# Performance work log

Measured on AMD Instinct MI355X. Metric: run time of the kernel, lower is better.

Reference implementation:

```python
import jax, jax.numpy as jnp
import numpy as np

H = 2048          # hidden size
N_HEADS = 16
HEAD_DIM = H // N_HEADS   # 128
ATTN_SCALE = 8.0          # attention_scale > 1.0 -> custom max-subtract path
B, S = 2, 2048


def setup_inputs() -> dict:
    key = jax.random.key(0)
    k1, k2, k3, k4, k5 = jax.random.split(key, 5)
    hidden_states = jax.random.normal(k1, (B, S, H), dtype=jnp.float32)
    # causal left-to-right multiplicative mask, broadcast over batch and heads
    ltor_mask = jnp.tril(jnp.ones((S, S), dtype=jnp.float32))[None, None]
    std = 0.02
    W_qkv = jax.random.normal(k2, (H, 3 * H), dtype=jnp.float32) * std
    b_qkv = jnp.zeros((3 * H,), dtype=jnp.float32)
    W_out = jax.random.normal(k3, (H, H), dtype=jnp.float32) * std
    b_out = jnp.zeros((H,), dtype=jnp.float32)
    return {"hidden_states": hidden_states, "ltor_mask": ltor_mask,
            "W_qkv": W_qkv, "b_qkv": b_qkv, "W_out": W_out, "b_out": b_out}


def reference(hidden_states, ltor_mask, W_qkv, b_qkv, W_out, b_out):
    b, s, h = hidden_states.shape
    # fused QKV projection: [b, s, 3h]
    qkv = jnp.einsum('bsh,hk->bsk', hidden_states, W_qkv) + b_qkv
    q, k, v = jnp.split(qkv, 3, axis=-1)
    # [b, s, h] -> [b, n, s, hn]
    def to_heads(t):
        return t.reshape(b, s, N_HEADS, HEAD_DIM).transpose(0, 2, 1, 3)
    q, k, v = to_heads(q), to_heads(k), to_heads(v)
    # custom scale: q / sqrt(scale), k / sqrt(hn * scale)
    inv = 1.0 / (ATTN_SCALE * np.sqrt(np.float32(HEAD_DIM)))
    scores = jnp.einsum('bnqd,bnkd->bnqk', q, k) * jnp.float32(inv)
    # multiplicative mask BEFORE max-subtract (zeroes masked positions)
    scores = scores * ltor_mask
    # attention_scale > 1.0 path: subtract row max, re-multiply by scale
    scores = (scores - jnp.max(scores, axis=-1, keepdims=True)) * jnp.float32(ATTN_SCALE)
    # additive large-negative fill on masked entries
    scores = scores + jnp.float32(-65504.0) * (1.0 - ltor_mask)
    probs = jax.nn.softmax(scores, axis=-1)
    ctx = jnp.einsum('bnqk,bnkd->bnqd', probs, v)
    ctx = ctx.transpose(0, 2, 1, 3).reshape(b, s, h)
    out = jnp.einsum('bsh,hk->bsk', ctx, W_out) + b_out
    return out
```

## Files before the change

### kernel.cpp

```cpp
#include <hip/hip_runtime.h>

#define S_LEN 2048
#define HDIM  2048
#define NHEADS 16
#define DHEAD 128
#define BATCH 2
#define MROWS (BATCH * S_LEN)
#define QKVN  (3 * HDIM)

typedef _Float16 f16;
typedef _Float16 f16x8 __attribute__((ext_vector_type(8)));
typedef _Float16 f16x4 __attribute__((ext_vector_type(4)));
typedef float    f32x4 __attribute__((ext_vector_type(4)));
typedef float    f32x16 __attribute__((ext_vector_type(16)));

typedef const __attribute__((address_space(1))) void* gas_ptr;
typedef __attribute__((address_space(3))) void*       las_ptr;

#define MFMA16(a, b, c)  __builtin_amdgcn_mfma_f32_16x16x32_f16(a, b, c, 0, 0, 0)
#define MFMA32(a, b, c)  __builtin_amdgcn_mfma_f32_32x32x16_f16(a, b, c, 0, 0, 0)

__device__ __forceinline__ void gl_lds16(const f16* g, f16* lds_wave_base) {
  __builtin_amdgcn_global_load_lds((gas_ptr)g, (las_ptr)lds_wave_base, 16, 0, 0);
}


__device__ __forceinline__ void transpose_tile(const float* __restrict__ W,
                                               f16* __restrict__ Wb,
                                               int K, int N, int k0, int n0,
                                               float* tile ) {
  int tr = threadIdx.x >> 4;
  int tc = (threadIdx.x & 15) * 4;
  int KT = K >> 5;
#pragma unroll
  for (int rr = 0; rr < 4; ++rr) {
    int r = rr * 16 + tr;
    float4 v = *(const float4*)(W + (size_t)(k0 + r) * N + n0 + tc);
    tile[r * 65 + tc + 0] = v.x; tile[r * 65 + tc + 1] = v.y;
    tile[r * 65 + tc + 2] = v.z; tile[r * 65 + tc + 3] = v.w;
  }
  __syncthreads();
#pragma unroll
  for (int rr = 0; rr < 4; ++rr) {
    int r = rr * 16 + tr;
    int n = n0 + r;
    int kBase = k0 + tc;
    f16x4 o;
#pragma unroll
    for (int c = 0; c < 4; ++c) o[c] = (f16)tile[(tc + c) * 65 + r];
    int nt = n >> 7, nn = n & 127;
    int kt = kBase >> 5, kc = (kBase >> 3) & 3, j = kBase & 7;
    *(f16x4*)(Wb + ((size_t)nt * KT + kt) * 4096 + (kc * 128 + nn) * 8 + j) = o;
  }
}

__global__ __launch_bounds__(256) void prep_kernel(const float* __restrict__ X,
                                                   f16* __restrict__ Xb,
                                                   const float* __restrict__ Wqkv,
                                                   f16* __restrict__ Wqkvb,
                                                   const float* __restrict__ Wout,
                                                   f16* __restrict__ Woutb) {
  __shared__ float tile[64 * 65];
  int bz = blockIdx.x;
  if (bz < 2048) {
    int kt = bz & 63, rt = bz >> 6;
    int t = threadIdx.x;
    int m = t >> 1, half = t & 1;
    const float* src = X + (size_t)(rt * 128 + m) * HDIM + kt * 32 + half * 16;
    float4 v0 = ((const float4*)src)[0];
    float4 v1 = ((const float4*)src)[1];
    float4 v2 = ((const float4*)src)[2];
    float4 v3 = ((const float4*)src)[3];
    f16x8 a = {(f16)v0.x, (f16)v0.y, (f16)v0.z, (f16)v0.w,
               (f16)v1.x, (f16)v1.y, (f16)v1.z, (f16)v1.w};
    f16x8 b = {(f16)v2.x, (f16)v2.y, (f16)v2.z, (f16)v2.w,
               (f16)v3.x, (f16)v3.y, (f16)v3.z, (f16)v3.w};
    f16* dst = Xb + ((size_t)rt * 64 + kt) * 4096 + ((half * 2) * 128 + m) * 8;
    *(f16x8*)dst = a;
    *(f16x8*)(dst + 1024) = b;
  } else if (bz < 5120) {
    int u = bz - 2048;
    int nx = u % 96, ky = u / 96;
    transpose_tile(Wqkv, Wqkvb, HDIM, QKVN, ky * 64, nx * 64, tile);
  } else {
    int u = bz - 5120;
    int nx = u & 31, ky = u >> 5;
    transpose_tile(Wout, Woutb, HDIM, HDIM, ky * 64, nx * 64, tile);
  }
}

__global__ __launch_bounds__(512, 2) void gemm_qkv_kernel(const f16* __restrict__ Ablk,
                                                          const f16* __restrict__ Bblk,
                                                          const float* __restrict__ bias,
                                                          f16* __restrict__ Qr,
                                                          f16* __restrict__ KB,
                                                          f16* __restrict__ VB) {
  __shared__ f16 As[3][2][4096];
  __shared__ f16 Bs[3][3][4096];
  const int tid = threadIdx.x;
  const int lane = tid & 63, wv = tid >> 6;
  const int lhi = lane >> 4, llo = lane & 15;
  const int wr = wv >> 2, wc = wv & 3;

  int lin = blockIdx.x + 16 * blockIdx.y;
  int xcd = lin & 7, slot = lin >> 3;
  int bx = (xcd & 3) * 4 + (slot & 3);
  int by = (xcd >> 2) * 8 + (slot >> 2);

  const int KT = HDIM >> 5;
  const f16* Ab0 = Ablk + (size_t)(2 * by)     * KT * 4096;
  const f16* Ab1 = Ablk + (size_t)(2 * by + 1) * KT * 4096;
  const f16* Bb0 = Bblk + (size_t)(3 * bx)     * KT * 4096;
  const f16* Bb1 = Bblk + (size_t)(3 * bx + 1) * KT * 4096;
  const f16* Bb2 = Bblk + (size_t)(3 * bx + 2) * KT * 4096;

  f32x4 acc[8][6];
#pragma unroll
  for (int i = 0; i < 8; ++i)
#pragma unroll
    for (int j = 0; j < 6; ++j) acc[i][j] = (f32x4){0.f, 0.f, 0.f, 0.f};

  auto stA = [&](int bufi, int kt) {
    gl_lds16(Ab0 + (size_t)kt * 4096 + tid * 8, &As[bufi][0][0] + wv * 512);
    gl_lds16(Ab1 + (size_t)kt * 4096 + tid * 8, &As[bufi][1][0] + wv * 512);
  };
  auto stB = [&](int bufi, int kt) {
    gl_lds16(Bb0 + (size_t)kt * 4096 + tid * 8, &Bs[bufi][0][0] + wv * 512);
    gl_lds16(Bb1 + (size_t)kt * 4096 + tid * 8, &Bs[bufi][1][0] + wv * 512);
    gl_lds16(Bb2 + (size_t)kt * 4096 + tid * 8, &Bs[bufi][2][0] + wv * 512);
  };
  auto rdB = [&](int bufi, int j) -> f16x8 {
    int cg = wc * 96 + j * 16;
    return *(const f16x8*)(&Bs[bufi][cg >> 7][0] + (lhi * 128 + (cg & 127) + llo) * 8);
  };

  stA(0, 0); stB(0, 0);
  stA(1, 1); stB(1, 1);

  for (int t = 0; t < KT; ++t) {
    const int buf = t % 3;
    const bool st = (t + 2 < KT);
    const int nb = (t + 2) % 3;

    if (t + 1 < KT) asm volatile("s_waitcnt vmcnt(5)" ::: "memory");
    else            asm volatile("s_waitcnt vmcnt(0)" ::: "memory");
    __builtin_amdgcn_s_barrier();

    const f16* Ah = &As[buf][wr][0];
    f16x8 afr[8], bA, bB;

#pragma unroll
    for (int i = 0; i < 8; ++i)
      afr[i] = *(const f16x8*)(Ah + (lhi * 128 + i * 16 + llo) * 8);
    bA = rdB(buf, 0); bB = rdB(buf, 1);
    if (st) stA(nb, t + 2);
    __builtin_amdgcn_s_barrier();
    asm volatile("s_waitcnt lgkmcnt(0)" ::: "memory");
    __builtin_amdgcn_s_setprio(1);
#pragma unroll
    for (int i = 0; i < 8; ++i) acc[i][0] = MFMA16(afr[i], bA, acc[i][0]);
#pragma unroll
    for (int i = 0; i < 8; ++i) acc[i][1] = MFMA16(afr[i], bB, acc[i][1]);
    __builtin_amdgcn_s_setprio(0);

    bA = rdB(buf, 2); bB = rdB(buf, 3);
    if (st) stB(nb, t + 2);
    __builtin_amdgcn_s_barrier();
    asm volatile("s_waitcnt lgkmcnt(0)" ::: "memory");
    __builtin_amdgcn_s_setprio(1);
#pragma unroll
    for (int i = 0; i < 8; ++i) acc[i][2] = MFMA16(afr[i], bA, acc[i][2]);
#pragma unroll
    for (int i = 0; i < 8; ++i) acc[i][3] = MFMA16(afr[i], bB, acc[i][3]);
    __builtin_amdgcn_s_setprio(0);

    bA = rdB(buf, 4); bB = rdB(buf, 5);
    __builtin_amdgcn_s_barrier();
    asm volatile("s_waitcnt lgkmcnt(0)" ::: "memory");
    __builtin_amdgcn_s_setprio(1);
#pragma unroll
    for (int i = 0; i < 8; ++i) acc[i][4] = MFMA16(afr[i], bA, acc[i][4]);
#pragma unroll
    for (int i = 0; i < 8; ++i) acc[i][5] = MFMA16(afr[i], bB, acc[i][5]);
    __builtin_amdgcn_s_setprio(0);
  }

#pragma unroll
  for (int j = 0; j < 6; ++j) {
    int col = bx * 384 + wc * 96 + j * 16 + llo;
    float bv = bias[col];
#pragma unroll
    for (int i = 0; i < 8; ++i) {
      int rowb = by * 256 + wr * 128 + i * 16 + lhi * 4;
      int region = col >> 11;
      if (region == 0) {
#pragma unroll
        for (int r = 0; r < 4; ++r)
          Qr[(size_t)(rowb + r) * HDIM + col] = (f16)(acc[i][j][r] + bv);
      } else if (region == 1) {
        int cK = col - HDIM;
        int hd = cK >> 7, d = cK & 127, g = d >> 3, dj = d & 7;
#pragma unroll
        for (int r = 0; r < 4; ++r) {
          int row = rowb + r;
          int b = row >> 11, s = row & 2047;
          int kt2 = s >> 6, key = s & 63;
          size_t addr = ((((size_t)(b * 16 + hd) * 32 + kt2) * 16 + g) * 64 + key) * 8 + dj;
          KB[addr] = (f16)(acc[i][j][r] + bv);
        }
      } else {
        int cV = col - 2 * HDIM;
        int hd = cV >> 7, d = cV & 127;
        int row = rowb;
        int b = row >> 11, s = row & 2047;
        int kt2 = s >> 6, key = s & 63;
        int kg = key >> 3, kj = key & 7;
        f16x4 pv = {(f16)(acc[i][j][0] + bv), (f16)(acc[i][j][1] + bv),
                    (f16)(acc[i][j][2] + bv), (f16)(acc[i][j][3] + bv)};
        size_t addr = ((((size_t)(b * 16 + hd) * 32 + kt2) * 8 + kg) * 128 + d) * 8 + kj;
        *(f16x4*)(VB + addr) = pv;
      }
    }
  }
}

__global__ __launch_bounds__(512, 2) void gemm_out_kernel(const f16* __restrict__ Ablk,
                                                          const f16* __restrict__ Bblk,
                                                          f16* __restrict__ Cpart) {
  __shared__ f16 As[4][2][4096];
  __shared__ f16 Bs[4][2][4096];
  const int tid = threadIdx.x;
  const int lane = tid & 63, wv = tid >> 6;
  const int lhi = lane >> 4, llo = lane & 15;
  const int wr = wv >> 2, wc = wv & 3;

  int lin = blockIdx.x + 8 * (blockIdx.y + 16 * blockIdx.z);
  int xcd = lin & 7, slot = lin >> 3;
  int bx = slot & 7;
  int by = (xcd >> 1) * 4 + (slot >> 3);
  int bz = xcd & 1;

  const int KT = HDIM >> 5;
  const int ntiles = KT >> 1;
  const int t0 = bz * ntiles;

  const f16* Ab0 = Ablk + ((size_t)(2 * by)     * KT + t0) * 4096;
  const f16* Ab1 = Ablk + ((size_t)(2 * by + 1) * KT + t0) * 4096;
  const f16* Bb0 = Bblk + ((size_t)(2 * bx)     * KT + t0) * 4096;
  const f16* Bb1 = Bblk + ((size_t)(2 * bx + 1) * KT + t0) * 4096;

  f32x4 acc[8][4];
#pragma unroll
  for (int i = 0; i < 8; ++i)
#pragma unroll
    for (int j = 0; j < 4; ++j) acc[i][j] = (f32x4){0.f, 0.f, 0.f, 0.f};

  auto stA = [&](int bufi, int kt) {
    gl_lds16(Ab0 + (size_t)kt * 4096 + tid * 8, &As[bufi][0][0] + wv * 512);
    gl_lds16(Ab1 + (size_t)kt * 4096 + tid * 8, &As[bufi][1][0] + wv * 512);
  };
  auto stB = [&](int bufi, int kt) {
    gl_lds16(Bb0 + (size_t)kt * 4096 + tid * 8, &Bs[bufi][0][0] + wv * 512);
    gl_lds16(Bb1 + (size_t)kt * 4096 + tid * 8, &Bs[bufi][1][0] + wv * 512);
  };

#pragma unroll
  for (int u = 0; u < 3; ++u) { stA(u, u); stB(u, u); }

  for (int t = 0; t < ntiles; ++t) {
    const int buf = t & 3;
    const bool st = (t + 3 < ntiles);
    const int nb = (t + 3) & 3, ntile = t + 3;

    if (t + 2 < ntiles)      asm volatile("s_waitcnt vmcnt(8)" ::: "memory");
    else if (t + 1 < ntiles) asm volatile("s_waitcnt vmcnt(4)" ::: "memory");
    else                     asm volatile("s_waitcnt vmcnt(0)" ::: "memory");
    __builtin_amdgcn_s_barrier();

    const f16* Ah = &As[buf][wr][0];
    const f16* Bh = &Bs[buf][wc >> 1][0];
    f16x8 bfr[4], afr[4];

#pragma unroll
    for (int j = 0; j < 4; ++j)
      bfr[j] = *(const f16x8*)(Bh + (lhi * 128 + (wc & 1) * 64 + j * 16 + llo) * 8);
#pragma unroll
    for (int i = 0; i < 4; ++i)
      afr[i] = *(const f16x8*)(Ah + (lhi * 128 + i * 16 + llo) * 8);
    if (st) stA(nb, ntile);
    __builtin_amdgcn_s_barrier();
    asm volatile("s_waitcnt lgkmcnt(0)" ::: "memory");
    __builtin_amdgcn_s_setprio(1);
#pragma unroll
    for (int i = 0; i < 4; ++i)
#pragma unroll
      for (int j = 0; j < 4; ++j) acc[i][j] = MFMA16(afr[i], bfr[j], acc[i][j]);
    __builtin_amdgcn_s_setprio(0);
    __builtin_amdgcn_s_barrier();

#pragma unroll
    for (int i = 0; i < 4; ++i)
      afr[i] = *(const f16x8*)(Ah + (lhi * 128 + (i + 4) * 16 + llo) * 8);
    if (st) stB(nb, ntile);
    __builtin_amdgcn_s_barrier();
    asm volatile("s_waitcnt lgkmcnt(0)" ::: "memory");
    __builtin_amdgcn_s_setprio(1);
#pragma unroll
    for (int i = 0; i < 4; ++i)
#pragma unroll
      for (int j = 0; j < 4; ++j) acc[i + 4][j] = MFMA16(afr[i], bfr[j], acc[i + 4][j]);
    __builtin_amdgcn_s_setprio(0);
  }

#pragma unroll
  for (int j = 0; j < 4; ++j) {
    int col = bx * 256 + wc * 64 + j * 16 + llo;
#pragma unroll
    for (int i = 0; i < 8; ++i) {
      int rowb = by * 256 + wr * 128 + i * 16 + lhi * 4;
      size_t zoff = (size_t)bz * MROWS * HDIM;
#pragma unroll
      for (int r = 0; r < 4; ++r)
        Cpart[zoff + (size_t)(rowb + r) * HDIM + col] = (f16)acc[i][j][r];
    }
  }
}

__global__ __launch_bounds__(256) void merge_out_kernel(const f16* __restrict__ Cpart,
                                                        const float* __restrict__ bias,
                                                        float* __restrict__ out) {
  int t = blockIdx.x * 256 + threadIdx.x;
  int col8 = (t & 255) * 8;
  int row = t >> 8;
  size_t base = (size_t)row * HDIM + col8;
  const size_t MN = (size_t)MROWS * HDIM;
  f16x8 a = *(const f16x8*)(Cpart + base);
  f16x8 b = *(const f16x8*)(Cpart + MN + base);
  float4 b0 = *(const float4*)(bias + col8);
  float4 b1 = *(const float4*)(bias + col8 + 4);
  float4 o0 = {(float)a[0] + (float)b[0] + b0.x, (float)a[1] + (float)b[1] + b0.y,
               (float)a[2] + (float)b[2] + b0.z, (float)a[3] + (float)b[3] + b0.w};
  float4 o1 = {(float)a[4] + (float)b[4] + b1.x, (float)a[5] + (float)b[5] + b1.y,
               (float)a[6] + (float)b[6] + b1.z, (float)a[7] + (float)b[7] + b1.w};
  *(float4*)(out + base) = o0;
  *(float4*)(out + base + 4) = o1;
}

__global__ __launch_bounds__(512, 1) void attn_kernel(const f16* __restrict__ Qr,
                                                      const f16* __restrict__ KB,
                                                      const f16* __restrict__ VB,
                                                      f16* __restrict__ CTXb) {
  __shared__ f16 Ks[2][1024 * 8];
  __shared__ f16 Vs[2][1024 * 8];
  __shared__ f16 Ps[8][32 * 72];

  int tid = threadIdx.x, lane = tid & 63, w = tid >> 6;
  int l5 = lane & 31, hl = lane >> 5;

  int lin = blockIdx.x + 8 * blockIdx.y;
  int xcd = lin & 7, slot = lin >> 3;
  int bh = xcd + 8 * (slot & 3);
  int pr = slot >> 2;
  int qt = (w < 4) ? pr : (15 - pr);
  int b = bh >> 4, hd = bh & 15;
  int ktmax = 32 - 2 * pr;

  int qbase = qt * 128 + (w & 3) * 32;
  int qrow = qbase + l5;

  const f16* qp = Qr + (size_t)(b * S_LEN + qrow) * HDIM + hd * DHEAD + hl * 8;
  f16x8 qf[8];
#pragma unroll
  for (int s8 = 0; s8 < 8; ++s8) qf[s8] = *(const f16x8*)(qp + s8 * 16);

  f32x16 oac[4];
#pragma unroll
  for (int mt = 0; mt < 4; ++mt)
#pragma unroll
    for (int r = 0; r < 16; ++r) oac[mt][r] = 0.f;
  float rs = 0.f;

  const float C1 = 0.12752747419986393f;
  const float C2 = 11.541560327111708f;

  const f16* KBb = KB + (size_t)bh * 32 * 8192;
  const f16* VBb = VB + (size_t)bh * 32 * 8192;

  auto stage = [&](int bi, int kt) {
    const f16* Kt = KBb + (size_t)kt * 8192;
    const f16* Vt = VBb + (size_t)kt * 8192;
#pragma unroll
    for (int c = 0; c < 2; ++c) {
      int u0 = w * 128 + c * 64;
      gl_lds16(Kt + (size_t)(u0 + lane) * 8, Ks[bi] + u0 * 8);
      gl_lds16(Vt + (size_t)(u0 + lane) * 8, Vs[bi] + u0 * 8);
    }
  };

  stage(0, 0);

  for (int kt = 0; kt < ktmax; ++kt) {
    int bi = kt & 1;
    asm volatile("s_waitcnt vmcnt(0)" ::: "memory");
    __builtin_amdgcn_s_barrier();
    if (kt + 1 < ktmax) stage(bi ^ 1, kt + 1);

    if (kt * 64 <= qbase + 31) {
      f32x16 sac[2];
#pragma unroll
      for (int mt = 0; mt < 2; ++mt)
#pragma unroll
        for (int r = 0; r < 16; ++r) sac[mt][r] = 0.f;
#pragma unroll
      for (int s8 = 0; s8 < 8; ++s8) {
#pragma unroll
        for (int mt = 0; mt < 2; ++mt) {
          f16x8 kf = *(const f16x8*)(Ks[bi] + ((s8 * 2 + hl) * 64 + mt * 32 + l5) * 8);
          sac[mt] = MFMA32(kf, qf[s8], sac[mt]);
        }
      }

      bool diag = (kt * 64 + 63 > qbase);
#pragma unroll
      for (int mt = 0; mt < 2; ++mt) {
#pragma unroll
        for (int g4 = 0; g4 < 4; ++g4) {
          f16x4 pk;
#pragma unroll
          for (int r = 0; r < 4; ++r) {
            int keyl = mt * 32 + g4 * 8 + hl * 4 + r;
            float p = __builtin_amdgcn_exp2f(fmaf(sac[mt][g4 * 4 + r], C1, -C2));
            if (diag && (kt * 64 + keyl > qrow)) p = 0.f;
            rs += p;
            pk[r] = (f16)p;
          }
          *(f16x4*)(&Ps[w][l5 * 72 + mt * 32 + g4 * 8 + hl * 4]) = pk;
        }
      }
      asm volatile("s_waitcnt lgkmcnt(0)" ::: "memory");

#pragma unroll
      for (int ks = 0; ks < 4; ++ks) {
        f16x8 pf = *(const f16x8*)(&Ps[w][l5 * 72 + ks * 16 + hl * 8]);
#pragma unroll
        for (int mt = 0; mt < 4; ++mt) {
          f16x8 vf = *(const f16x8*)(Vs[bi] + ((ks * 2 + hl) * 128 + mt * 32 + l5) * 8);
          oac[mt] = MFMA32(vf, pf, oac[mt]);
        }
      }
    }
  }

  float lsum = rs + __shfl_xor(rs, 32, 64);
  float inv = 1.0f / lsum;
  int row = b * S_LEN + qrow;
  int rt = row >> 7, rr = row & 127;
#pragma unroll
  for (int mt = 0; mt < 4; ++mt) {
#pragma unroll
    for (int g4 = 0; g4 < 4; ++g4) {
      int d = mt * 32 + g4 * 8 + hl * 4;
      int col = hd * DHEAD + d;
      f16x4 ov = {(f16)(oac[mt][g4 * 4 + 0] * inv), (f16)(oac[mt][g4 * 4 + 1] * inv),
                  (f16)(oac[mt][g4 * 4 + 2] * inv), (f16)(oac[mt][g4 * 4 + 3] * inv)};
      *(f16x4*)(CTXb + ((size_t)rt * 64 + (col >> 5)) * 4096 +
                (((col >> 3) & 3) * 128 + rr) * 8 + (col & 7)) = ov;
    }
  }
}

extern "C" void kernel_launch(void* const* d_in, const int* in_sizes, int n_in,
                              void* d_out, int out_size, void* d_ws, size_t ws_size,
                              hipStream_t stream) {
  const float* X    = (const float*)d_in[0];
  const float* Wqkv = (const float*)d_in[2];
  const float* bqkv = (const float*)d_in[3];
  const float* Wout = (const float*)d_in[4];
  const float* bout = (const float*)d_in[5];
  float* out = (float*)d_out;

  char* ws = (char*)d_ws;
  f16* Xb    = (f16*)ws;  ws += (size_t)MROWS * HDIM * sizeof(f16);
  f16* Wqkvb = (f16*)ws;  ws += (size_t)QKVN * HDIM * sizeof(f16);
  f16* Woutb = (f16*)ws;  ws += (size_t)HDIM * HDIM * sizeof(f16);
  f16* Qr    = (f16*)ws;  ws += (size_t)MROWS * HDIM * sizeof(f16);
  f16* KB    = (f16*)ws;  ws += (size_t)32 * 32 * 8192 * sizeof(f16);
  f16* VB    = (f16*)ws;  ws += (size_t)32 * 32 * 8192 * sizeof(f16);
  f16* Cpart = (f16*)ws;  ws += (size_t)2 * MROWS * HDIM * sizeof(f16);
  f16* CTXb  = Xb;

  prep_kernel<<<6144, 256, 0, stream>>>(X, Xb, Wqkv, Wqkvb, Wout, Woutb);

  gemm_qkv_kernel<<<dim3(QKVN / 384, MROWS / 256), 512, 0, stream>>>(
      Xb, Wqkvb, bqkv, Qr, KB, VB);

  attn_kernel<<<dim3(8, 32), 512, 0, stream>>>(Qr, KB, VB, CTXb);

  gemm_out_kernel<<<dim3(HDIM / 256, MROWS / 256, 2), 512, 0, stream>>>(
      CTXb, Woutb, Cpart);

  merge_out_kernel<<<(MROWS * HDIM / 8) / 256, 256, 0, stream>>>(Cpart, bout, out);
}
```

Baseline: 368.2 us.

## Replace split-K output GEMM with narrower tiles and fuse bias epilogue

The output projection previously used a split-K of two with 256x256 tiles, writing f16 partials that a separate merge kernel summed with the bias. It now uses 256x128 tiles over the full K range and writes fp32 output plus bias directly, so the merge kernel and the partial buffer are gone. The launch still has 256 blocks, but each does half the N-width, which lowers per-block reuse of A. It removes one kernel launch and roughly 32 MB of partial-buffer traffic, and the partial results are no longer rounded to f16 before the final sum.

```diff
diff --git a/kernel.cpp b/kernel.cpp
--- a/kernel.cpp
+++ b/kernel.cpp
@@ -226,124 +226,85 @@
 
 __global__ __launch_bounds__(512, 2) void gemm_out_kernel(const f16* __restrict__ Ablk,
                                                           const f16* __restrict__ Bblk,
-                                                          f16* __restrict__ Cpart) {
+                                                          const float* __restrict__ bias,
+                                                          float* __restrict__ out) {
   __shared__ f16 As[4][2][4096];
-  __shared__ f16 Bs[4][2][4096];
+  __shared__ f16 Bs[4][4096];
   const int tid = threadIdx.x;
   const int lane = tid & 63, wv = tid >> 6;
   const int lhi = lane >> 4, llo = lane & 15;
   const int wr = wv >> 2, wc = wv & 3;
 
-  int lin = blockIdx.x + 8 * (blockIdx.y + 16 * blockIdx.z);
+  int lin = blockIdx.x + 16 * blockIdx.y;
   int xcd = lin & 7, slot = lin >> 3;
-  int bx = slot & 7;
-  int by = (xcd >> 1) * 4 + (slot >> 3);
-  int bz = xcd & 1;
+  int bx = (xcd & 3) * 4 + (slot & 3);
+  int by = (xcd >> 2) * 8 + (slot >> 2);
 
   const int KT = HDIM >> 5;
-  const int ntiles = KT >> 1;
-  const int t0 = bz * ntiles;
-
-  const f16* Ab0 = Ablk + ((size_t)(2 * by)     * KT + t0) * 4096;
-  const f16* Ab1 = Ablk + ((size_t)(2 * by + 1) * KT + t0) * 4096;
-  const f16* Bb0 = Bblk + ((size_t)(2 * bx)     * KT + t0) * 4096;
-  const f16* Bb1 = Bblk + ((size_t)(2 * bx + 1) * KT + t0) * 4096;
-
-  f32x4 acc[8][4];
+  const f16* Ab0 = Ablk + (size_t)(2 * by)     * KT * 4096;
+  const f16* Ab1 = Ablk + (size_t)(2 * by + 1) * KT * 4096;
+  const f16* Bb0 = Bblk + (size_t)bx * KT * 4096;
+
+  f32x4 acc[8][2];
 #pragma unroll
   for (int i = 0; i < 8; ++i)
 #pragma unroll
-    for (int j = 0; j < 4; ++j) acc[i][j] = (f32x4){0.f, 0.f, 0.f, 0.f};
+    for (int j = 0; j < 2; ++j) acc[i][j] = (f32x4){0.f, 0.f, 0.f, 0.f};
 
   auto stA = [&](int bufi, int kt) {
     gl_lds16(Ab0 + (size_t)kt * 4096 + tid * 8, &As[bufi][0][0] + wv * 512);
     gl_lds16(Ab1 + (size_t)kt * 4096 + tid * 8, &As[bufi][1][0] + wv * 512);
   };
   auto stB = [&](int bufi, int kt) {
-    gl_lds16(Bb0 + (size_t)kt * 4096 + tid * 8, &Bs[bufi][0][0] + wv * 512);
-    gl_lds16(Bb1 + (size_t)kt * 4096 + tid * 8, &Bs[bufi][1][0] + wv * 512);
+    gl_lds16(Bb0 + (size_t)kt * 4096 + tid * 8, &Bs[bufi][0] + wv * 512);
   };
 
 #pragma unroll
   for (int u = 0; u < 3; ++u) { stA(u, u); stB(u, u); }
 
-  for (int t = 0; t < ntiles; ++t) {
+  for (int t = 0; t < KT; ++t) {
     const int buf = t & 3;
-    const bool st = (t + 3 < ntiles);
+    const bool st = (t + 3 < KT);
     const int nb = (t + 3) & 3, ntile = t + 3;
 
-    if (t + 2 < ntiles)      asm volatile("s_waitcnt vmcnt(8)" ::: "memory");
-    else if (t + 1 < ntiles) asm volatile("s_waitcnt vmcnt(4)" ::: "memory");
-    else                     asm volatile("s_waitcnt vmcnt(0)" ::: "memory");
+    if (t + 2 < KT)      asm volatile("s_waitcnt vmcnt(6)" ::: "memory");
+    else if (t + 1 < KT) asm volatile("s_waitcnt vmcnt(3)" ::: "memory");
+    else                 asm volatile("s_waitcnt vmcnt(0)" ::: "memory");
     __builtin_amdgcn_s_barrier();
 
     const f16* Ah = &As[buf][wr][0];
-    const f16* Bh = &Bs[buf][wc >> 1][0];
-    f16x8 bfr[4], afr[4];
-
-#pragma unroll
-    for (int j = 0; j < 4; ++j)
-      bfr[j] = *(const f16x8*)(Bh + (lhi * 128 + (wc & 1) * 64 + j * 16 + llo) * 8);
-#pragma unroll
-    for (int i = 0; i < 4; ++i)
+    f16x8 afr[8], bfr[2];
+
+#pragma unroll
+    for (int i = 0; i < 8; ++i)
       afr[i] = *(const f16x8*)(Ah + (lhi * 128 + i * 16 + llo) * 8);
-    if (st) stA(nb, ntile);
+#pragma unroll
+    for (int j = 0; j < 2; ++j)
+      bfr[j] = *(const f16x8*)(Bs[buf] + (lhi * 128 + wc * 32 + j * 16 + llo) * 8);
+    if (st) { stA(nb, ntile); stB(nb, ntile); }
     __builtin_amdgcn_s_barrier();
     asm volatile("s_waitcnt lgkmcnt(0)" ::: "memory");
     __builtin_amdgcn_s_setprio(1);
 #pragma unroll
-    for (int i = 0; i < 4; ++i)
-#pragma unroll
-      for (int j = 0; j < 4; ++j) acc[i][j] = MFMA16(afr[i], bfr[j], acc[i][j]);
+    for (int i = 0; i < 8; ++i) {
+      acc[i][0] = MFMA16(afr[i], bfr[0], acc[i][0]);
+      acc[i][1] = MFMA16(afr[i], bfr[1], acc[i][1]);
+    }
     __builtin_amdgcn_s_setprio(0);
-    __builtin_amdgcn_s_barrier();
-
-#pragma unroll
-    for (int i = 0; i < 4; ++i)
-      afr[i] = *(const f16x8*)(Ah + (lhi * 128 + (i + 4) * 16 + llo) * 8);
-    if (st) stB(nb, ntile);
-    __builtin_amdgcn_s_barrier();
-    asm volatile("s_waitcnt lgkmcnt(0)" ::: "memory");
-    __builtin_amdgcn_s_setprio(1);
-#pragma unroll
-    for (int i = 0; i < 4; ++i)
-#pragma unroll
-      for (int j = 0; j < 4; ++j) acc[i + 4][j] = MFMA16(afr[i], bfr[j], acc[i + 4][j]);
-    __builtin_amdgcn_s_setprio(0);
-  }
-
-#pragma unroll
-  for (int j = 0; j < 4; ++j) {
-    int col = bx * 256 + wc * 64 + j * 16 + llo;
+  }
+
+#pragma unroll
+  for (int j = 0; j < 2; ++j) {
+    int col = bx * 128 + wc * 32 + j * 16 + llo;
+    float bv = bias[col];
 #pragma unroll
     for (int i = 0; i < 8; ++i) {
       int rowb = by * 256 + wr * 128 + i * 16 + lhi * 4;
-      size_t zoff = (size_t)bz * MROWS * HDIM;
 #pragma unroll
       for (int r = 0; r < 4; ++r)
-        Cpart[zoff + (size_t)(rowb + r) * HDIM + col] = (f16)acc[i][j][r];
-    }
-  }
-}
-
-__global__ __launch_bounds__(256) void merge_out_kernel(const f16* __restrict__ Cpart,
-                                                        const float* __restrict__ bias,
-                                                        float* __restrict__ out) {
-  int t = blockIdx.x * 256 + threadIdx.x;
-  int col8 = (t & 255) * 8;
-  int row = t >> 8;
-  size_t base = (size_t)row * HDIM + col8;
-  const size_t MN = (size_t)MROWS * HDIM;
-  f16x8 a = *(const f16x8*)(Cpart + base);
-  f16x8 b = *(const f16x8*)(Cpart + MN + base);
-  float4 b0 = *(const float4*)(bias + col8);
-  float4 b1 = *(const float4*)(bias + col8 + 4);
-  float4 o0 = {(float)a[0] + (float)b[0] + b0.x, (float)a[1] + (float)b[1] + b0.y,
-               (float)a[2] + (float)b[2] + b0.z, (float)a[3] + (float)b[3] + b0.w};
-  float4 o1 = {(float)a[4] + (float)b[4] + b1.x, (float)a[5] + (float)b[5] + b1.y,
-               (float)a[6] + (float)b[6] + b1.z, (float)a[7] + (float)b[7] + b1.w};
-  *(float4*)(out + base) = o0;
-  *(float4*)(out + base + 4) = o1;
+        out[(size_t)(rowb + r) * HDIM + col] = acc[i][j][r] + bv;
+    }
+  }
 }
 
 __global__ __launch_bounds__(512, 1) void attn_kernel(const f16* __restrict__ Qr,
@@ -486,7 +447,6 @@
   f16* Qr    = (f16*)ws;  ws += (size_t)MROWS * HDIM * sizeof(f16);
   f16* KB    = (f16*)ws;  ws += (size_t)32 * 32 * 8192 * sizeof(f16);
   f16* VB    = (f16*)ws;  ws += (size_t)32 * 32 * 8192 * sizeof(f16);
-  f16* Cpart = (f16*)ws;  ws += (size_t)2 * MROWS * HDIM * sizeof(f16);
   f16* CTXb  = Xb;
 
   prep_kernel<<<6144, 256, 0, stream>>>(X, Xb, Wqkv, Wqkvb, Wout, Woutb);
@@ -496,8 +456,6 @@
 
   attn_kernel<<<dim3(8, 32), 512, 0, stream>>>(Qr, KB, VB, CTXb);
 
-  gemm_out_kernel<<<dim3(HDIM / 256, MROWS / 256, 2), 512, 0, stream>>>(
-      CTXb, Woutb, Cpart);
-
-  merge_out_kernel<<<(MROWS * HDIM / 8) / 256, 256, 0, stream>>>(Cpart, bout, out);
-}
+  gemm_out_kernel<<<dim3(HDIM / 128, MROWS / 256), 512, 0, stream>>>(
+      CTXb, Woutb, bout, out);
+}
```

New measurement: 368.6 us. About the same (+0.1%).
